# Performance work log

Hardware: AMD Instinct MI355X
Metric: run time of the kernel (lower is better)

## Reference

```python
import jax, jax.numpy as jnp
import numpy as np

THRESHOLD = 0.5
SLACK = 3
EPS = 1e-12
B, H, W = 16, 512, 512


def _shift(p, dy, dx, b, h, w):
    # p is zero-padded by 1 on spatial dims; returns neighbor at offset (dy, dx)
    return p[:, 1 + dy:1 + dy + h, 1 + dx:1 + dx + w]


def _thin_sub(img, step):
    # One Zhang-Suen sub-iteration on bool image [B,H,W] (zero boundary, as skimage)
    b, h, w = img.shape
    p = jnp.pad(img.astype(jnp.int32), ((0, 0), (1, 1), (1, 1)))
    # P2..P9 clockwise starting at North
    P2 = _shift(p, -1, 0, b, h, w); P3 = _shift(p, -1, 1, b, h, w)
    P4 = _shift(p, 0, 1, b, h, w);  P5 = _shift(p, 1, 1, b, h, w)
    P6 = _shift(p, 1, 0, b, h, w);  P7 = _shift(p, 1, -1, b, h, w)
    P8 = _shift(p, 0, -1, b, h, w); P9 = _shift(p, -1, -1, b, h, w)
    seq = [P2, P3, P4, P5, P6, P7, P8, P9, P2]
    Bn = P2 + P3 + P4 + P5 + P6 + P7 + P8 + P9          # neighbor count
    A = sum((1 - seq[k]) * seq[k + 1] for k in range(8))  # 0->1 transitions
    cond = (Bn >= 2) & (Bn <= 6) & (A == 1)
    if step == 0:
        cond = cond & (P2 * P4 * P6 == 0) & (P4 * P6 * P8 == 0)
    else:
        cond = cond & (P2 * P4 * P8 == 0) & (P2 * P6 * P8 == 0)
    return img & ~cond


def _skeletonize(img):
    # Iterate Zhang-Suen thinning to convergence (skimage.morphology.skeletonize 2D = Zhang's method)
    def body(state):
        cur, _ = state
        nxt = _thin_sub(_thin_sub(cur, 0), 1)
        return (nxt, jnp.any(nxt != cur))

    out, _ = jax.lax.while_loop(lambda s: s[1], body, (img, jnp.array(True)))
    return out


def _edt_sq(mask):
    # Exact squared Euclidean distance to nearest True pixel, separable 2-pass.
    b, h, w = mask.shape
    BIG = h + w  # larger than any attainable 1D distance
    g = jnp.where(mask, 0, BIG).astype(jnp.int32)  # [B,H,W]

    # pass 1: 1D nearest-True distance along rows (axis=1) via fwd/bwd scans
    def fscan(carry, row):
        d = jnp.minimum(row, carry + 1)
        return d, d

    g_rows = jnp.moveaxis(g, 1, 0)  # [H,B,W]
    init = jnp.full((b, w), BIG, jnp.int32)
    _, fwd = jax.lax.scan(fscan, init, g_rows)
    _, bwd = jax.lax.scan(fscan, init, g_rows[::-1])
    f = jnp.minimum(jnp.minimum(fwd, bwd[::-1]), BIG)  # [H,B,W]
    f2 = jnp.moveaxis(f * f, 0, 1)  # [B,H,W] squared vertical distance

    # pass 2: d2[b,i,j] = min_{j'} f2[b,i,j'] + (j-j')^2 (lower envelope, memory-friendly lax.map)
    js = jnp.arange(w, dtype=jnp.int32)

    def one_col(j):
        off = (js - j) ** 2  # [W]
        return jnp.min(f2 + off[None, None, :], axis=-1)  # [B,H]

    d2 = jax.lax.map(one_col, js)  # [W,B,H]
    return jnp.transpose(d2, (1, 2, 0))  # [B,H,W]


def setup_inputs() -> dict:
    key = jax.random.key(0)
    k1, k2 = jax.random.split(key)
    y_pred = jax.random.uniform(k1, (B, H, W), dtype=jnp.float32)
    y_true = jax.random.uniform(k2, (B, H, W), dtype=jnp.float32)
    return {"y_pred": y_pred, "y_true": y_true}


def reference(y_pred, y_true):
    p = y_pred > THRESHOLD  # greater_is_road=True binarization
    g = y_true > THRESHOLD
    p = _skeletonize(p)
    g = _skeletonize(g)
    d2_gt = _edt_sq(g)   # EDT of ~g == distance to nearest g pixel
    d2_pr = _edt_sq(p)
    s2 = SLACK * SLACK   # dist <= slack  <=>  dist^2 <= slack^2 (integer sq EDT)
    tp_area = d2_gt <= s2
    fp_area = ~tp_area
    fn_area = d2_pr > s2
    ax = (1, 2)
    TP = jnp.sum(tp_area & p, ax).astype(jnp.float32)
    FP = jnp.sum(fp_area & p, ax).astype(jnp.float32)
    FN = jnp.sum(fn_area & g, ax).astype(jnp.float32)
    correctness = TP / (TP + FP + EPS)
    completeness = TP / (TP + FN + EPS)
    quality = TP / (TP + FP + FN + EPS)
    # mean over batch -> [3]: [correctness, completeness, quality]
    return jnp.mean(jnp.stack([correctness, completeness, quality], axis=1), axis=0)
```

## Files before the change

kernel.cpp:

```cpp
#include <hip/hip_runtime.h>
#include <stdint.h>

#define HH 512
#define WW 512
#define HW (HH * WW)
#define WPR 8
#define NWORDS (HH * WPR)
#define NTHREADS 1024
#define WPT (NWORDS / NTHREADS)
#define NB 16

typedef unsigned long long u64;

__device__ __forceinline__ u64 ldw(const u64* M, int r, int c) {
    return (r < 0 || r >= HH || c < 0 || c >= WPR) ? 0ULL : M[r * WPR + c];
}

__device__ __forceinline__ u64 zs_word(const u64* M, u64 cc, int r, int c, int step) {
    u64 nm = ldw(M, r - 1, c - 1), nc = ldw(M, r - 1, c), np = ldw(M, r - 1, c + 1);
    u64 cm = ldw(M, r,     c - 1),                        cp = ldw(M, r,     c + 1);
    u64 sm = ldw(M, r + 1, c - 1), sc = ldw(M, r + 1, c), sp = ldw(M, r + 1, c + 1);

    u64 P2 = nc;
    u64 P3 = (nc >> 1) | (np << 63);
    u64 P4 = (cc >> 1) | (cp << 63);
    u64 P5 = (sc >> 1) | (sp << 63);
    u64 P6 = sc;
    u64 P7 = (sc << 1) | (sm >> 63);
    u64 P8 = (cc << 1) | (cm >> 63);
    u64 P9 = (nc << 1) | (nm >> 63);

    u64 ab = P2 ^ P3;
    u64 s1 = ab ^ P4, c1 = (P2 & P3) | (ab & P4);
    u64 de = P5 ^ P6;
    u64 s2 = de ^ P7, c2 = (P5 & P6) | (de & P7);
    u64 s3 = P8 ^ P9, c3 = P8 & P9;
    u64 gh = s1 ^ s2;
    u64 b0 = gh ^ s3, c4 = (s1 & s2) | (gh & s3);
    u64 ij = c1 ^ c2;
    u64 s4 = ij ^ c3, c5 = (c1 & c2) | (ij & c3);
    u64 b1 = s4 ^ c4, c6 = s4 & c4;
    u64 b2 = c5 ^ c6, b3 = c5 & c6;

    u64 Bge2 = b1 | b2 | b3;
    u64 Ble6 = ~(b3 | (b2 & b1 & b0));

    u64 a1, a2, t;
    t = ~P2 & P3; a1 = t; a2 = 0ULL;
    t = ~P3 & P4; a2 |= a1 & t; a1 |= t;
    t = ~P4 & P5; a2 |= a1 & t; a1 |= t;
    t = ~P5 & P6; a2 |= a1 & t; a1 |= t;
    t = ~P6 & P7; a2 |= a1 & t; a1 |= t;
    t = ~P7 & P8; a2 |= a1 & t; a1 |= t;
    t = ~P8 & P9; a2 |= a1 & t; a1 |= t;
    t = ~P9 & P2; a2 |= a1 & t; a1 |= t;
    u64 Aeq1 = a1 & ~a2;

    u64 sccond;
    if (step == 0) sccond = ~(P2 & P4 & P6) & ~(P4 & P6 & P8);
    else           sccond = ~(P2 & P4 & P8) & ~(P2 & P6 & P8);

    return cc & ~(Bge2 & Ble6 & Aeq1 & sccond);
}

__global__ __launch_bounds__(256)
void pack_kernel(const float* __restrict__ y_pred,
                 const float* __restrict__ y_true,
                 u64* __restrict__ bits ,
                 int* __restrict__ cnt ) {
    int tid = threadIdx.x;
    if (blockIdx.x == 0 && tid < 4 * NB) cnt[tid] = 0;

    int t = blockIdx.x * 256 + tid;
    size_t g0 = (size_t)t * 16;
    const float* src;
    size_t off;
    if (g0 < (size_t)NB * HW) { src = y_pred; off = g0; }
    else                      { src = y_true; off = g0 - (size_t)NB * HW; }
    const float4* s4 = (const float4*)(src + off);
    float4 a = s4[0];
    float4 b = s4[1];
    float4 c = s4[2];
    float4 d = s4[3];
    unsigned m =
        ((unsigned)(a.x > 0.5f) << 0)  | ((unsigned)(a.y > 0.5f) << 1)  |
        ((unsigned)(a.z > 0.5f) << 2)  | ((unsigned)(a.w > 0.5f) << 3)  |
        ((unsigned)(b.x > 0.5f) << 4)  | ((unsigned)(b.y > 0.5f) << 5)  |
        ((unsigned)(b.z > 0.5f) << 6)  | ((unsigned)(b.w > 0.5f) << 7)  |
        ((unsigned)(c.x > 0.5f) << 8)  | ((unsigned)(c.y > 0.5f) << 9)  |
        ((unsigned)(c.z > 0.5f) << 10) | ((unsigned)(c.w > 0.5f) << 11) |
        ((unsigned)(d.x > 0.5f) << 12) | ((unsigned)(d.y > 0.5f) << 13) |
        ((unsigned)(d.z > 0.5f) << 14) | ((unsigned)(d.w > 0.5f) << 15);
    ((unsigned short*)bits)[t] = (unsigned short)m;
}

__global__ __launch_bounds__(NTHREADS)
void skel_kernel(u64* __restrict__ bits ) {
    __shared__ u64 Mb[2][NWORDS];
    __shared__ unsigned int Cpb[2][HH + 2];
    __shared__ int s_any[3];

    int bx = blockIdx.x;
    int tid = threadIdx.x;
    int lane = tid & 63;

    u64* gm = bits + (size_t)bx * NWORDS;

    {
        const ulonglong2* s2 = (const ulonglong2*)gm;
        ulonglong2* m2 = (ulonglong2*)Mb[0];
        #pragma unroll
        for (int k = 0; k < 2; ++k) {
            int i = k * NTHREADS + tid;
            m2[i] = s2[i];
        }
    }

    for (int i = tid; i < HH + 2; i += NTHREADS) {
        Cpb[0][i] = (i >= 1 && i <= HH) ? 0x1FEu : 0u;
        Cpb[1][i] = 0u;
    }
    if (tid < 3) s_any[tid] = 0;

    unsigned dl[WPT];
    #pragma unroll
    for (int k = 0; k < WPT; ++k) dl[k] = 0x1FEu;

    int it = 0;
    bool done = false;
    for (;;) {
        for (int step = 0; step < 2; ++step) {
            __syncthreads();
            if (step == 0 && it > 0) {
                if (s_any[(it + 2) % 3] == 0) { done = true; break; }
            }
            const u64* Ms = Mb[step];
            u64* Md = Mb[step ^ 1];
            const unsigned* CpS = Cpb[step];
            unsigned* CpD = Cpb[step ^ 1];
            bool anyc = false;
            #pragma unroll
            for (int k = 0; k < WPT; ++k) {
                int wi = k * NTHREADS + tid;
                int r = wi >> 3, c = wi & 7;
                unsigned need = ((CpS[r] | CpS[r + 1] | CpS[r + 2]) >> c) & 7u;
                u64 cur = Ms[wi];
                u64 x = cur;
                bool chg = false;
                if (need) {
                    x = zs_word(Ms, cur, r, c, step);
                    chg = (x != cur);
                }
                Md[wi] = x;
                u64 bal = __ballot(chg);
                anyc |= (bal != 0);
                if ((lane & 7) == 0) {
                    unsigned byte = ((unsigned)(bal >> lane) & 0xFFu) << 1;
                    CpD[(wi >> 3) + 1] = byte | dl[k];
                    dl[k] = byte;
                }
            }
            if (anyc) s_any[it % 3] = 1;
            if (step == 1 && tid == 0) s_any[(it + 1) % 3] = 0;
        }
        if (done) break;
        ++it;
    }

    {
        ulonglong2* d2 = (ulonglong2*)gm;
        const ulonglong2* m2 = (const ulonglong2*)Mb[0];
        #pragma unroll
        for (int k = 0; k < 2; ++k) {
            int i = k * NTHREADS + tid;
            d2[i] = m2[i];
        }
    }
}

#define STRIPS 8
#define SROWS (HH / STRIPS)
#define SR2 (SROWS + 6)

__device__ __forceinline__ u64 ldws(const u64* M, int r, int c) {
    return (c < 0 || c >= WPR) ? 0ULL : M[r * WPR + c];
}

__device__ __forceinline__ u64 dil3s(const u64* M, int r, int c) {
    u64 cm = ldws(M, r, c - 1), cc = ldws(M, r, c), cp = ldws(M, r, c + 1);
    u64 h = cc
          | (cc >> 1) | (cp << 63)
          | (cc >> 2) | (cp << 62)
          | (cc >> 3) | (cp << 61)
          | (cc << 1) | (cm >> 63)
          | (cc << 2) | (cm >> 62)
          | (cc << 3) | (cm >> 61);
    u64 um = ldws(M, r - 1, c - 1) | ldws(M, r + 1, c - 1) | ldws(M, r - 2, c - 1) | ldws(M, r + 2, c - 1);
    u64 uc = ldws(M, r - 1, c    ) | ldws(M, r + 1, c    ) | ldws(M, r - 2, c    ) | ldws(M, r + 2, c    );
    u64 up = ldws(M, r - 1, c + 1) | ldws(M, r + 1, c + 1) | ldws(M, r - 2, c + 1) | ldws(M, r + 2, c + 1);
    h |= uc
       | (uc >> 1) | (up << 63)
       | (uc >> 2) | (up << 62)
       | (uc << 1) | (um >> 63)
       | (uc << 2) | (um >> 62);
    h |= ldws(M, r - 3, c) | ldws(M, r + 3, c);
    return h;
}

__global__ __launch_bounds__(256)
void count_kernel(const u64* __restrict__ skel, int* __restrict__ cnt) {
    __shared__ u64 P[SR2 * WPR];
    __shared__ u64 G[SR2 * WPR];
    __shared__ int acc[4];

    int b = blockIdx.x / STRIPS;
    int s = blockIdx.x % STRIPS;
    int tid = threadIdx.x;
    int r0 = s * SROWS - 3;

    const u64* sp = skel + (size_t)b * NWORDS;
    const u64* sg = skel + (size_t)(NB + b) * NWORDS;
    for (int i = tid; i < SR2 * WPR; i += 256) {
        int gr = r0 + (i >> 3);
        bool in = (gr >= 0 && gr < HH);
        int gi = gr * WPR + (i & 7);
        P[i] = in ? sp[gi] : 0ULL;
        G[i] = in ? sg[gi] : 0ULL;
    }
    if (tid < 4) acc[tid] = 0;
    __syncthreads();

    int cp = 0, cg = 0, tp = 0, fnh = 0;
    #pragma unroll
    for (int k = 0; k < 2; ++k) {
        int w = k * 256 + tid;
        int r = (w >> 3) + 3, c = w & 7;
        u64 pw = P[r * WPR + c], gw = G[r * WPR + c];
        cp  += __popcll(pw);
        cg  += __popcll(gw);
        tp  += __popcll(pw & dil3s(G, r, c));
        fnh += __popcll(gw & dil3s(P, r, c));
    }
    #pragma unroll
    for (int o = 32; o > 0; o >>= 1) {
        cp  += __shfl_down(cp, o);
        cg  += __shfl_down(cg, o);
        tp  += __shfl_down(tp, o);
        fnh += __shfl_down(fnh, o);
    }
    if ((tid & 63) == 0) {
        atomicAdd(&acc[0], cp);
        atomicAdd(&acc[1], cg);
        atomicAdd(&acc[2], tp);
        atomicAdd(&acc[3], fnh);
    }
    __syncthreads();
    if (tid < 4) atomicAdd(&cnt[b * 4 + tid], acc[tid]);
}

__global__ void ccq_reduce(const int* __restrict__ cnt, float* __restrict__ out) {
    int k = threadIdx.x;
    if (k < 3) {
        float s = 0.0f;
        for (int b = 0; b < NB; ++b) {
            float TP = (float)cnt[b * 4 + 2];
            float FP = (float)(cnt[b * 4 + 0] - cnt[b * 4 + 2]);
            float FN = (float)(cnt[b * 4 + 1] - cnt[b * 4 + 3]);
            float v = (k == 0) ? TP / (TP + FP + 1e-12f)
                    : (k == 1) ? TP / (TP + FN + 1e-12f)
                               : TP / (TP + FP + FN + 1e-12f);
            s += v;
        }
        out[k] = s * (1.0f / NB);
    }
}

extern "C" void kernel_launch(void* const* d_in, const int* in_sizes, int n_in,
                              void* d_out, int out_size, void* d_ws, size_t ws_size,
                              hipStream_t stream) {
    (void)in_sizes; (void)n_in; (void)out_size; (void)ws_size;
    const float* y_pred = (const float*)d_in[0];
    const float* y_true = (const float*)d_in[1];
    float* out = (float*)d_out;

    u64* bits = (u64*)d_ws;
    int* cnt = (int*)((char*)d_ws + (size_t)2 * NB * NWORDS * sizeof(u64));

    hipLaunchKernelGGL(pack_kernel, dim3(2 * NB * HW / 16 / 256), dim3(256), 0, stream,
                       y_pred, y_true, bits, cnt);
    hipLaunchKernelGGL(skel_kernel, dim3(2 * NB), dim3(NTHREADS), 0, stream, bits);
    hipLaunchKernelGGL(count_kernel, dim3(NB * STRIPS), dim3(256), 0, stream,
                       bits, cnt);
    hipLaunchKernelGGL(ccq_reduce, dim3(1), dim3(64), 0, stream, cnt, out);
}
```

Before: 115.7 us.

## Fuse counting and final reduction into skeleton kernel via pairwise completion flags

The count and reduce kernels are folded into the skeletonization kernel. Whichever block of a pred/gt pair finishes second loads its partner's skeleton into shared memory, computes the dilated overlap counts, and the last pair to finish computes the final metrics. This removes two kernel launches and a global re-read of the skeletons. It also skips shared-memory writes for words whose value did not change in the current or previous step. In exchange, the counting work runs on only 16 blocks instead of 128, and correctness depends on atomic flags and thread fences.

```diff
diff --git a/kernel.cpp b/kernel.cpp
--- a/kernel.cpp
+++ b/kernel.cpp
@@ -63,13 +63,34 @@
     return cc & ~(Bge2 & Ble6 & Aeq1 & sccond);
 }
 
+__device__ __forceinline__ u64 dil3f(const u64* M, int r, int c) {
+    u64 cm = ldw(M, r, c - 1), cc = ldw(M, r, c), cp = ldw(M, r, c + 1);
+    u64 h = cc
+          | (cc >> 1) | (cp << 63)
+          | (cc >> 2) | (cp << 62)
+          | (cc >> 3) | (cp << 61)
+          | (cc << 1) | (cm >> 63)
+          | (cc << 2) | (cm >> 62)
+          | (cc << 3) | (cm >> 61);
+    u64 um = ldw(M, r - 1, c - 1) | ldw(M, r + 1, c - 1) | ldw(M, r - 2, c - 1) | ldw(M, r + 2, c - 1);
+    u64 uc = ldw(M, r - 1, c    ) | ldw(M, r + 1, c    ) | ldw(M, r - 2, c    ) | ldw(M, r + 2, c    );
+    u64 up = ldw(M, r - 1, c + 1) | ldw(M, r + 1, c + 1) | ldw(M, r - 2, c + 1) | ldw(M, r + 2, c + 1);
+    h |= uc
+       | (uc >> 1) | (up << 63)
+       | (uc >> 2) | (up << 62)
+       | (uc << 1) | (um >> 63)
+       | (uc << 2) | (um >> 62);
+    h |= ldw(M, r - 3, c) | ldw(M, r + 3, c);
+    return h;
+}
+
 __global__ __launch_bounds__(256)
 void pack_kernel(const float* __restrict__ y_pred,
                  const float* __restrict__ y_true,
                  u64* __restrict__ bits ,
                  int* __restrict__ cnt ) {
     int tid = threadIdx.x;
-    if (blockIdx.x == 0 && tid < 4 * NB) cnt[tid] = 0;
+    if (blockIdx.x == 0 && tid < 4 * NB + 17) cnt[tid] = 0;
 
     int t = blockIdx.x * 256 + tid;
     size_t g0 = (size_t)t * 16;
@@ -95,10 +116,14 @@
 }
 
 __global__ __launch_bounds__(NTHREADS)
-void skel_kernel(u64* __restrict__ bits ) {
+void skel_kernel(u64* __restrict__ bits ,
+                 int* __restrict__ cnt, int* __restrict__ pairflag,
+                 int* __restrict__ done2, float* __restrict__ out) {
     __shared__ u64 Mb[2][NWORDS];
     __shared__ unsigned int Cpb[2][HH + 2];
     __shared__ int s_any[3];
+    __shared__ int s_role;
+    __shared__ int s_acc[4];
 
     int bx = blockIdx.x;
     int tid = threadIdx.x;
@@ -121,10 +146,12 @@
         Cpb[1][i] = 0u;
     }
     if (tid < 3) s_any[tid] = 0;
+    if (tid < 4) s_acc[tid] = 0;
 
     unsigned dl[WPT];
+    u64 balPrev[WPT];
     #pragma unroll
-    for (int k = 0; k < WPT; ++k) dl[k] = 0x1FEu;
+    for (int k = 0; k < WPT; ++k) { dl[k] = 0x1FEu; balPrev[k] = ~0ULL; }
 
     int it = 0;
     bool done = false;
@@ -151,9 +178,10 @@
                     x = zs_word(Ms, cur, r, c, step);
                     chg = (x != cur);
                 }
-                Md[wi] = x;
                 u64 bal = __ballot(chg);
                 anyc |= (bal != 0);
+                if (((bal | balPrev[k]) >> lane) & 1) Md[wi] = x;
+                balPrev[k] = bal;
                 if ((lane & 7) == 0) {
                     unsigned byte = ((unsigned)(bal >> lane) & 0xFFu) << 1;
                     CpD[(wi >> 3) + 1] = byte | dl[k];
@@ -176,70 +204,38 @@
             d2[i] = m2[i];
         }
     }
-}
-
-#define STRIPS 8
-#define SROWS (HH / STRIPS)
-#define SR2 (SROWS + 6)
-
-__device__ __forceinline__ u64 ldws(const u64* M, int r, int c) {
-    return (c < 0 || c >= WPR) ? 0ULL : M[r * WPR + c];
-}
-
-__device__ __forceinline__ u64 dil3s(const u64* M, int r, int c) {
-    u64 cm = ldws(M, r, c - 1), cc = ldws(M, r, c), cp = ldws(M, r, c + 1);
-    u64 h = cc
-          | (cc >> 1) | (cp << 63)
-          | (cc >> 2) | (cp << 62)
-          | (cc >> 3) | (cp << 61)
-          | (cc << 1) | (cm >> 63)
-          | (cc << 2) | (cm >> 62)
-          | (cc << 3) | (cm >> 61);
-    u64 um = ldws(M, r - 1, c - 1) | ldws(M, r + 1, c - 1) | ldws(M, r - 2, c - 1) | ldws(M, r + 2, c - 1);
-    u64 uc = ldws(M, r - 1, c    ) | ldws(M, r + 1, c    ) | ldws(M, r - 2, c    ) | ldws(M, r + 2, c    );
-    u64 up = ldws(M, r - 1, c + 1) | ldws(M, r + 1, c + 1) | ldws(M, r - 2, c + 1) | ldws(M, r + 2, c + 1);
-    h |= uc
-       | (uc >> 1) | (up << 63)
-       | (uc >> 2) | (up << 62)
-       | (uc << 1) | (um >> 63)
-       | (uc << 2) | (um >> 62);
-    h |= ldws(M, r - 3, c) | ldws(M, r + 3, c);
-    return h;
-}
-
-__global__ __launch_bounds__(256)
-void count_kernel(const u64* __restrict__ skel, int* __restrict__ cnt) {
-    __shared__ u64 P[SR2 * WPR];
-    __shared__ u64 G[SR2 * WPR];
-    __shared__ int acc[4];
-
-    int b = blockIdx.x / STRIPS;
-    int s = blockIdx.x % STRIPS;
-    int tid = threadIdx.x;
-    int r0 = s * SROWS - 3;
-
-    const u64* sp = skel + (size_t)b * NWORDS;
-    const u64* sg = skel + (size_t)(NB + b) * NWORDS;
-    for (int i = tid; i < SR2 * WPR; i += 256) {
-        int gr = r0 + (i >> 3);
-        bool in = (gr >= 0 && gr < HH);
-        int gi = gr * WPR + (i & 7);
-        P[i] = in ? sp[gi] : 0ULL;
-        G[i] = in ? sg[gi] : 0ULL;
-    }
-    if (tid < 4) acc[tid] = 0;
-    __syncthreads();
+    __syncthreads();
+    if (tid == 0) {
+        __threadfence();
+        s_role = atomicAdd(&pairflag[bx & (NB - 1)], 1);
+    }
+    __syncthreads();
+    if (s_role == 0) return;
+    __threadfence();
+
+    {
+        const ulonglong2* p2 = (const ulonglong2*)(bits + (size_t)(bx ^ NB) * NWORDS);
+        ulonglong2* m2 = (ulonglong2*)Mb[1];
+        #pragma unroll
+        for (int k = 0; k < 2; ++k) {
+            int i = k * NTHREADS + tid;
+            m2[i] = p2[i];
+        }
+    }
+    __syncthreads();
+    const u64* P = (bx < NB) ? Mb[0] : Mb[1];
+    const u64* G = (bx < NB) ? Mb[1] : Mb[0];
 
     int cp = 0, cg = 0, tp = 0, fnh = 0;
     #pragma unroll
-    for (int k = 0; k < 2; ++k) {
-        int w = k * 256 + tid;
-        int r = (w >> 3) + 3, c = w & 7;
-        u64 pw = P[r * WPR + c], gw = G[r * WPR + c];
+    for (int k = 0; k < WPT; ++k) {
+        int wi = k * NTHREADS + tid;
+        int r = wi >> 3, c = wi & 7;
+        u64 pw = P[wi], gw = G[wi];
         cp  += __popcll(pw);
         cg  += __popcll(gw);
-        tp  += __popcll(pw & dil3s(G, r, c));
-        fnh += __popcll(gw & dil3s(P, r, c));
+        tp  += __popcll(pw & dil3f(G, r, c));
+        fnh += __popcll(gw & dil3f(P, r, c));
     }
     #pragma unroll
     for (int o = 32; o > 0; o >>= 1) {
@@ -248,30 +244,39 @@
         tp  += __shfl_down(tp, o);
         fnh += __shfl_down(fnh, o);
     }
-    if ((tid & 63) == 0) {
-        atomicAdd(&acc[0], cp);
-        atomicAdd(&acc[1], cg);
-        atomicAdd(&acc[2], tp);
-        atomicAdd(&acc[3], fnh);
-    }
-    __syncthreads();
-    if (tid < 4) atomicAdd(&cnt[b * 4 + tid], acc[tid]);
-}
-
-__global__ void ccq_reduce(const int* __restrict__ cnt, float* __restrict__ out) {
-    int k = threadIdx.x;
-    if (k < 3) {
+    if (lane == 0) {
+        atomicAdd(&s_acc[0], cp);
+        atomicAdd(&s_acc[1], cg);
+        atomicAdd(&s_acc[2], tp);
+        atomicAdd(&s_acc[3], fnh);
+    }
+    __syncthreads();
+    int b = bx & (NB - 1);
+    if (tid < 4) atomicAdd(&cnt[b * 4 + tid], s_acc[tid]);
+    __syncthreads();
+    if (tid == 0) {
+        __threadfence();
+        s_role = (atomicAdd(done2, 1) == NB - 1) ? 2 : 0;
+    }
+    __syncthreads();
+    if (s_role != 2) return;
+    __threadfence();
+
+    if (tid < 3) {
         float s = 0.0f;
-        for (int b = 0; b < NB; ++b) {
-            float TP = (float)cnt[b * 4 + 2];
-            float FP = (float)(cnt[b * 4 + 0] - cnt[b * 4 + 2]);
-            float FN = (float)(cnt[b * 4 + 1] - cnt[b * 4 + 3]);
-            float v = (k == 0) ? TP / (TP + FP + 1e-12f)
-                    : (k == 1) ? TP / (TP + FN + 1e-12f)
-                               : TP / (TP + FP + FN + 1e-12f);
+        for (int i = 0; i < NB; ++i) {
+            float c0 = (float)atomicAdd(&cnt[i * 4 + 0], 0);
+            float c1 = (float)atomicAdd(&cnt[i * 4 + 1], 0);
+            float TP = (float)atomicAdd(&cnt[i * 4 + 2], 0);
+            float c3 = (float)atomicAdd(&cnt[i * 4 + 3], 0);
+            float FP = c0 - TP;
+            float FN = c1 - c3;
+            float v = (tid == 0) ? TP / (TP + FP + 1e-12f)
+                    : (tid == 1) ? TP / (TP + FN + 1e-12f)
+                                 : TP / (TP + FP + FN + 1e-12f);
             s += v;
         }
-        out[k] = s * (1.0f / NB);
+        out[tid] = s * (1.0f / NB);
     }
 }
 
@@ -285,11 +290,11 @@
 
     u64* bits = (u64*)d_ws;
     int* cnt = (int*)((char*)d_ws + (size_t)2 * NB * NWORDS * sizeof(u64));
+    int* pairflag = cnt + 4 * NB;
+    int* done2 = cnt + 4 * NB + 16;
 
     hipLaunchKernelGGL(pack_kernel, dim3(2 * NB * HW / 16 / 256), dim3(256), 0, stream,
                        y_pred, y_true, bits, cnt);
-    hipLaunchKernelGGL(skel_kernel, dim3(2 * NB), dim3(NTHREADS), 0, stream, bits);
-    hipLaunchKernelGGL(count_kernel, dim3(NB * STRIPS), dim3(256), 0, stream,
-                       bits, cnt);
-    hipLaunchKernelGGL(ccq_reduce, dim3(1), dim3(64), 0, stream, cnt, out);
-}
+    hipLaunchKernelGGL(skel_kernel, dim3(2 * NB), dim3(NTHREADS), 0, stream,
+                       bits, cnt, pairflag, done2, out);
+}
```

Measured after the change: 180.0 us. +55.5%, slower.

## Restructure skeletonize kernel with padded LDS tiles and per-thread 4-row column strips

Applied to the files above, without the earlier changes.

Each thread now processes a vertical strip of four consecutive words in one column instead of two words spread far apart. This lets it reuse the north and south neighbour rows through a sliding register window. Shared memory gets a zero-padded halo (stride 10, with extra border rows), which removes the per-load bounds checks. It also skips the core evaluation for all-zero words, writes the destination only when this or the previous pass changed, and tracks change flags per 4-row block. Risks are the extra LDS footprint, possible bank conflicts from the stride-10 layout, and an added iteration cap.

```diff
diff --git a/kernel.cpp b/kernel.cpp
--- a/kernel.cpp
+++ b/kernel.cpp
@@ -7,29 +7,16 @@
 #define WPR 8
 #define NWORDS (HH * WPR)
 #define NTHREADS 1024
-#define WPT (NWORDS / NTHREADS)
 #define NB 16
 
+#define LSTR 10
+#define LROWS (HH + 2)
+#define LWORDS (LROWS * LSTR)
+
 typedef unsigned long long u64;
 
-__device__ __forceinline__ u64 ldw(const u64* M, int r, int c) {
-    return (r < 0 || r >= HH || c < 0 || c >= WPR) ? 0ULL : M[r * WPR + c];
-}
-
-__device__ __forceinline__ u64 zs_word(const u64* M, u64 cc, int r, int c, int step) {
-    u64 nm = ldw(M, r - 1, c - 1), nc = ldw(M, r - 1, c), np = ldw(M, r - 1, c + 1);
-    u64 cm = ldw(M, r,     c - 1),                        cp = ldw(M, r,     c + 1);
-    u64 sm = ldw(M, r + 1, c - 1), sc = ldw(M, r + 1, c), sp = ldw(M, r + 1, c + 1);
-
-    u64 P2 = nc;
-    u64 P3 = (nc >> 1) | (np << 63);
-    u64 P4 = (cc >> 1) | (cp << 63);
-    u64 P5 = (sc >> 1) | (sp << 63);
-    u64 P6 = sc;
-    u64 P7 = (sc << 1) | (sm >> 63);
-    u64 P8 = (cc << 1) | (cm >> 63);
-    u64 P9 = (nc << 1) | (nm >> 63);
-
+__device__ __forceinline__ u64 zs_core(u64 cc, u64 P2, u64 P3, u64 P4, u64 P5,
+                                       u64 P6, u64 P7, u64 P8, u64 P9, int step) {
     u64 ab = P2 ^ P3;
     u64 s1 = ab ^ P4, c1 = (P2 & P3) | (ab & P4);
     u64 de = P5 ^ P6;
@@ -56,9 +43,8 @@
     t = ~P9 & P2; a2 |= a1 & t; a1 |= t;
     u64 Aeq1 = a1 & ~a2;
 
-    u64 sccond;
-    if (step == 0) sccond = ~(P2 & P4 & P6) & ~(P4 & P6 & P8);
-    else           sccond = ~(P2 & P4 & P8) & ~(P2 & P6 & P8);
+    u64 sccond = (step == 0) ? ~((P4 & P6) & (P2 | P8))
+                             : ~((P2 & P8) & (P4 | P6));
 
     return cc & ~(Bge2 & Ble6 & Aeq1 & sccond);
 }
@@ -94,37 +80,54 @@
     ((unsigned short*)bits)[t] = (unsigned short)m;
 }
 
-__global__ __launch_bounds__(NTHREADS)
+__global__ __launch_bounds__(NTHREADS, 4)
 void skel_kernel(u64* __restrict__ bits ) {
-    __shared__ u64 Mb[2][NWORDS];
-    __shared__ unsigned int Cpb[2][HH + 2];
+    __shared__ u64 Mb[2][LWORDS];
+    __shared__ unsigned int Cpb[2][130];
     __shared__ int s_any[3];
 
     int bx = blockIdx.x;
     int tid = threadIdx.x;
     int lane = tid & 63;
+    int c = tid & 7;
+    int rb = tid >> 3;
 
     u64* gm = bits + (size_t)bx * NWORDS;
+
+    if (tid < LROWS) {
+        int i = tid;
+        if (i == 0 || i == LROWS - 1) {
+            #pragma unroll
+            for (int j = 0; j < LSTR; ++j) { Mb[0][i * LSTR + j] = 0; Mb[1][i * LSTR + j] = 0; }
+        } else {
+            Mb[0][i * LSTR + 0] = 0; Mb[0][i * LSTR + 9] = 0;
+            Mb[1][i * LSTR + 0] = 0; Mb[1][i * LSTR + 9] = 0;
+        }
+    }
 
     {
         const ulonglong2* s2 = (const ulonglong2*)gm;
-        ulonglong2* m2 = (ulonglong2*)Mb[0];
         #pragma unroll
         for (int k = 0; k < 2; ++k) {
             int i = k * NTHREADS + tid;
-            m2[i] = s2[i];
-        }
-    }
-
-    for (int i = tid; i < HH + 2; i += NTHREADS) {
-        Cpb[0][i] = (i >= 1 && i <= HH) ? 0x1FEu : 0u;
-        Cpb[1][i] = 0u;
+            ulonglong2 v = s2[i];
+            int wi = i * 2;
+            int r = wi >> 3, c2 = wi & 7;
+            int li = (r + 1) * LSTR + c2 + 1;
+            Mb[0][li] = v.x;
+            Mb[0][li + 1] = v.y;
+        }
+    }
+
+    if (tid < 130) {
+        Cpb[0][tid] = (tid >= 1 && tid <= 128) ? 0x1FEu : 0u;
+        Cpb[1][tid] = 0u;
     }
     if (tid < 3) s_any[tid] = 0;
 
-    unsigned dl[WPT];
-    #pragma unroll
-    for (int k = 0; k < WPT; ++k) dl[k] = 0x1FEu;
+    unsigned dl = 0x1FEu;
+    bool prevchg = true;
+    int base = (rb * 4 + 1) * LSTR + (c + 1);
 
     int it = 0;
     bool done = false;
@@ -138,42 +141,77 @@
             u64* Md = Mb[step ^ 1];
             const unsigned* CpS = Cpb[step];
             unsigned* CpD = Cpb[step ^ 1];
-            bool anyc = false;
-            #pragma unroll
-            for (int k = 0; k < WPT; ++k) {
-                int wi = k * NTHREADS + tid;
-                int r = wi >> 3, c = wi & 7;
-                unsigned need = ((CpS[r] | CpS[r + 1] | CpS[r + 2]) >> c) & 7u;
-                u64 cur = Ms[wi];
-                u64 x = cur;
-                bool chg = false;
-                if (need) {
-                    x = zs_word(Ms, cur, r, c, step);
-                    chg = (x != cur);
-                }
-                Md[wi] = x;
-                u64 bal = __ballot(chg);
-                anyc |= (bal != 0);
-                if ((lane & 7) == 0) {
-                    unsigned byte = ((unsigned)(bal >> lane) & 0xFFu) << 1;
-                    CpD[(wi >> 3) + 1] = byte | dl[k];
-                    dl[k] = byte;
+
+            unsigned need = ((CpS[rb] | CpS[rb + 1] | CpS[rb + 2]) >> c) & 7u;
+            bool chg = false;
+            if (need) {
+                u64 Ca, Ea, Wa, Cb, Eb, Wb, Cc, Ec, Wc;
+                {   int a = base - LSTR;
+                    u64 x = Ms[a], mm = Ms[a - 1], pp = Ms[a + 1];
+                    Ca = x; Ea = (x >> 1) | (pp << 63); Wa = (x << 1) | (mm >> 63); }
+                {   int a = base;
+                    u64 x = Ms[a], mm = Ms[a - 1], pp = Ms[a + 1];
+                    Cb = x; Eb = (x >> 1) | (pp << 63); Wb = (x << 1) | (mm >> 63); }
+                u64 nv0 = 0, nv1 = 0, nv2 = 0, nv3 = 0;
+
+                {   int a = base + LSTR;
+                    u64 x = Ms[a], mm = Ms[a - 1], pp = Ms[a + 1];
+                    Cc = x; Ec = (x >> 1) | (pp << 63); Wc = (x << 1) | (mm >> 63);
+                    if (Cb) nv0 = zs_core(Cb, Ca, Ea, Eb, Ec, Cc, Wc, Wb, Wa, step);
+                    chg |= (nv0 != Cb);
+                    Ca = Cb; Ea = Eb; Wa = Wb; Cb = Cc; Eb = Ec; Wb = Wc; }
+                {   int a = base + 2 * LSTR;
+                    u64 x = Ms[a], mm = Ms[a - 1], pp = Ms[a + 1];
+                    Cc = x; Ec = (x >> 1) | (pp << 63); Wc = (x << 1) | (mm >> 63);
+                    if (Cb) nv1 = zs_core(Cb, Ca, Ea, Eb, Ec, Cc, Wc, Wb, Wa, step);
+                    chg |= (nv1 != Cb);
+                    Ca = Cb; Ea = Eb; Wa = Wb; Cb = Cc; Eb = Ec; Wb = Wc; }
+                {   int a = base + 3 * LSTR;
+                    u64 x = Ms[a], mm = Ms[a - 1], pp = Ms[a + 1];
+                    Cc = x; Ec = (x >> 1) | (pp << 63); Wc = (x << 1) | (mm >> 63);
+                    if (Cb) nv2 = zs_core(Cb, Ca, Ea, Eb, Ec, Cc, Wc, Wb, Wa, step);
+                    chg |= (nv2 != Cb);
+                    Ca = Cb; Ea = Eb; Wa = Wb; Cb = Cc; Eb = Ec; Wb = Wc; }
+                {   int a = base + 4 * LSTR;
+                    u64 x = Ms[a], mm = Ms[a - 1], pp = Ms[a + 1];
+                    Cc = x; Ec = (x >> 1) | (pp << 63); Wc = (x << 1) | (mm >> 63);
+                    if (Cb) nv3 = zs_core(Cb, Ca, Ea, Eb, Ec, Cc, Wc, Wb, Wa, step);
+                    chg |= (nv3 != Cb); }
+
+                if (chg | prevchg) {
+                    Md[base] = nv0;
+                    Md[base + LSTR] = nv1;
+                    Md[base + 2 * LSTR] = nv2;
+                    Md[base + 3 * LSTR] = nv3;
                 }
             }
-            if (anyc) s_any[it % 3] = 1;
+            prevchg = chg;
+
+            u64 bal = __ballot(chg);
+            if (bal && lane == 0) s_any[it % 3] = 1;
+            if ((lane & 7) == 0) {
+                unsigned byte = ((unsigned)(bal >> lane) & 0xFFu) << 1;
+                CpD[rb + 1] = byte | dl;
+                dl = byte;
+            }
             if (step == 1 && tid == 0) s_any[(it + 1) % 3] = 0;
         }
-        if (done) break;
+        if (done || it >= 1024) break;
         ++it;
     }
 
     {
         ulonglong2* d2 = (ulonglong2*)gm;
-        const ulonglong2* m2 = (const ulonglong2*)Mb[0];
         #pragma unroll
         for (int k = 0; k < 2; ++k) {
             int i = k * NTHREADS + tid;
-            d2[i] = m2[i];
+            int wi = i * 2;
+            int r = wi >> 3, c2 = wi & 7;
+            int li = (r + 1) * LSTR + c2 + 1;
+            ulonglong2 v;
+            v.x = Mb[0][li];
+            v.y = Mb[0][li + 1];
+            d2[i] = v;
         }
     }
 }
```

Result: no change. 115.9 us (+0.2%).
